# Optimization experiments

Hardware: AMD Instinct MI355X
Metric: run time of the kernel (lower is better)

The kernel has to match this reference:

```python
import jax, jax.numpy as jnp
import numpy as np

D_MODEL = 1024; D_STATE = 64; D_CONV = 4; EXPAND = 2; HEADDIM = 128; NGROUPS = 1; CHUNK = 256
D_INNER = EXPAND * D_MODEL            # 2048
NHEADS = D_INNER // HEADDIM           # 16
CONV_DIM = D_INNER + 2 * NGROUPS * D_STATE   # 2176
D_IN_PROJ = 2 * D_INNER + 2 * NGROUPS * D_STATE + NHEADS  # 4240
B = 4; G = 256; L = 2048
EPS = 1e-5


def setup_inputs() -> dict:
    key = jax.random.key(0)
    ks = jax.random.split(key, 12)
    def nrm(k, shape, s=0.02):
        return jax.random.normal(k, shape, jnp.float32) * s
    return dict(
        local_repr=jax.random.normal(ks[0], (B, L, D_MODEL), jnp.float32),
        global_repr=jax.random.normal(ks[1], (B, G, D_MODEL), jnp.float32),
        norm1_w=jnp.ones((D_MODEL,), jnp.float32), norm1_b=jnp.zeros((D_MODEL,), jnp.float32),
        norm2_w=jnp.ones((D_MODEL,), jnp.float32), norm2_b=jnp.zeros((D_MODEL,), jnp.float32),
        norm3_w=jnp.ones((D_MODEL,), jnp.float32), norm3_b=jnp.zeros((D_MODEL,), jnp.float32),
        in_proj_w=nrm(ks[2], (D_IN_PROJ, D_MODEL)),
        conv_w=nrm(ks[3], (CONV_DIM, D_CONV), 0.2),
        conv_b=jnp.zeros((CONV_DIM,), jnp.float32),
        dt_bias=jnp.log(jnp.expm1(jax.random.uniform(ks[4], (NHEADS,), jnp.float32, 1e-3, 0.1))),
        A_log=jnp.log(jax.random.uniform(ks[5], (NHEADS,), jnp.float32, 1.0, 16.0)),
        D_skip=jnp.ones((NHEADS,), jnp.float32),
        ssd_norm_w=jnp.ones((D_INNER,), jnp.float32),
        out_proj_w=nrm(ks[6], (D_MODEL, D_INNER)),
        ffn_w1=nrm(ks[7], (D_MODEL // 2, D_MODEL)),
        ffn_b1=jnp.zeros((D_MODEL // 2,), jnp.float32),
        ffn_w2=nrm(ks[8], (D_MODEL, D_MODEL // 2)),
        ffn_b2=jnp.zeros((D_MODEL,), jnp.float32),
    )


def _ln(x, w, b):
    mu = jnp.mean(x, axis=-1, keepdims=True)
    var = jnp.mean((x - mu) ** 2, axis=-1, keepdims=True)
    return (x - mu) * jax.lax.rsqrt(var + EPS) * w + b


def _segsum(a):
    # a: (..., T) -> (..., T, T) lower-triangular sums a[j+1..i]
    T = a.shape[-1]
    cs = jnp.cumsum(a, axis=-1)
    diff = cs[..., :, None] - cs[..., None, :]
    mask = jnp.tril(jnp.ones((T, T), bool))
    return jnp.where(mask, diff, -jnp.inf)


def _ssd(xdt, a_dt, Bh, Ch):
    # xdt: (b,t,h,p) = x*dt ; a_dt: (b,t,h) = dt*A ; Bh,Ch: (b,t,h,n)
    b, t, h, p = xdt.shape
    n = Bh.shape[-1]
    c = t // CHUNK
    X = xdt.reshape(b, c, CHUNK, h, p)
    Bc = Bh.reshape(b, c, CHUNK, h, n)
    Cc = Ch.reshape(b, c, CHUNK, h, n)
    Ac = a_dt.reshape(b, c, CHUNK, h).transpose(0, 3, 1, 2)  # (b,h,c,k)
    A_cum = jnp.cumsum(Ac, axis=-1)
    Lm = jnp.exp(_segsum(Ac))                                # (b,h,c,k,k)
    Y_diag = jnp.einsum('bckhn,bcshn,bhcks,bcshp->bckhp', Cc, Bc, Lm, X)
    decay_states = jnp.exp(A_cum[..., -1:] - A_cum)          # (b,h,c,k)
    states = jnp.einsum('bckhn,bhck,bckhp->bchpn', Bc, decay_states, X)
    A_last = jnp.pad(A_cum[..., -1], ((0, 0), (0, 0), (1, 0)))
    decay_chunk = jnp.exp(_segsum(A_last))                   # (b,h,c+1,c+1)
    states = jnp.concatenate([jnp.zeros_like(states[:, :1]), states], axis=1)
    new_states = jnp.einsum('bhzc,bchpn->bzhpn', decay_chunk, states)
    states_in = new_states[:, :-1]                           # (b,c,h,p,n)
    out_decay = jnp.exp(A_cum)                               # (b,h,c,k)
    Y_off = jnp.einsum('bckhn,bchpn,bhck->bckhp', Cc, states_in, out_decay)
    return (Y_diag + Y_off).reshape(b, t, h, p)


def _mamba2(x, in_proj_w, conv_w, conv_b, dt_bias, A_log, D_skip, ssd_norm_w, out_proj_w):
    b, t, _ = x.shape
    zxbcdt = x @ in_proj_w.T                                  # (b,t,D_IN_PROJ)
    z = zxbcdt[..., :D_INNER]
    xBC = zxbcdt[..., D_INNER:D_INNER + CONV_DIM]
    dt = jax.nn.softplus(zxbcdt[..., D_INNER + CONV_DIM:] + dt_bias)  # (b,t,h)
    # causal depthwise conv1d, kernel D_CONV
    xp = jnp.pad(xBC, ((0, 0), (D_CONV - 1, 0), (0, 0)))
    xBC = sum(xp[:, i:i + t, :] * conv_w[:, i] for i in range(D_CONV)) + conv_b
    xBC = jax.nn.silu(xBC)
    xs = xBC[..., :D_INNER].reshape(b, t, NHEADS, HEADDIM)
    Bm = xBC[..., D_INNER:D_INNER + NGROUPS * D_STATE].reshape(b, t, NGROUPS, D_STATE)
    Cm = xBC[..., D_INNER + NGROUPS * D_STATE:].reshape(b, t, NGROUPS, D_STATE)
    rep = NHEADS // NGROUPS
    Bh = jnp.repeat(Bm, rep, axis=2)
    Ch = jnp.repeat(Cm, rep, axis=2)
    A = -jnp.exp(A_log)                                       # (h,)
    Y = _ssd(xs * dt[..., None], dt * A, Bh, Ch)
    y = Y + D_skip[None, None, :, None] * xs
    y = y.reshape(b, t, D_INNER)
    # gated RMSNorm (norm_before_gate=False)
    y = y * jax.nn.silu(z)
    y = y * jax.lax.rsqrt(jnp.mean(y * y, axis=-1, keepdims=True) + EPS) * ssd_norm_w
    return y @ out_proj_w.T


def reference(local_repr, global_repr, norm1_w, norm1_b, norm2_w, norm2_b, norm3_w, norm3_b,
              in_proj_w, conv_w, conv_b, dt_bias, A_log, D_skip, ssd_norm_w, out_proj_w,
              ffn_w1, ffn_b1, ffn_w2, ffn_b2):
    local_n = _ln(local_repr, norm1_w, norm1_b)
    global_n = _ln(global_repr, norm2_w, norm2_b)
    x = jnp.concatenate([global_n, local_n], axis=1)          # (B, G+L, D)
    x = _mamba2(x, in_proj_w, conv_w, conv_b, dt_bias, A_log, D_skip, ssd_norm_w, out_proj_w)
    x = x[:, -local_n.shape[1]:, :] + local_n
    x = _ln(x, norm3_w, norm3_b)
    h = jax.nn.gelu(x @ ffn_w1.T + ffn_b1, approximate=False)
    return (h @ ffn_w2.T + ffn_b2) + x
```

## Files before the change

kernel.cpp:

```cpp
#include <hip/hip_runtime.h>
#include <math.h>

#define B_ 4
#define L_ 2048
#define G_ 256
#define T_ 2304
#define DM 1024
#define DINNER 2048
#define NH 16
#define HD 128
#define NSTATE 64
#define CONVD 2176
#define DPROJ 4240
#define NPROJ_PAD 4352
#define NCHUNK 9
#define CK 256
#define EPSV 1e-5f
#define CROWS 16
#define CONVBLKS 612

typedef unsigned short bf16t;
using bf16x8 = __attribute__((ext_vector_type(8))) short;
using f32x4  = __attribute__((ext_vector_type(4))) float;

__device__ __forceinline__ float bf2f(bf16t u) {
  return __uint_as_float(((unsigned int)u) << 16);
}
__device__ __forceinline__ bf16t f2bf(float f) {
  unsigned int u = __float_as_uint(f);
  u += 0x7FFFu + ((u >> 16) & 1u);
  return (bf16t)(u >> 16);
}

__device__ __forceinline__ void g2lds16(const bf16t* g, short* l) {
  __builtin_amdgcn_global_load_lds(
      (const __attribute__((address_space(1))) unsigned int*)g,
      (__attribute__((address_space(3))) unsigned int*)l, 16, 0, 0);
}

__device__ __forceinline__ int2 xcd_swz(int tiles_n) {
  int gx = gridDim.x, gy = gridDim.y;
  int id = blockIdx.y * gx + blockIdx.x;
  int cpx = (gx * gy) >> 3;
  int L = (id & 7) * cpx + (id >> 3);
  return make_int2(L % tiles_n, L / tiles_n);
}

__device__ __forceinline__ float2 block_reduce2(float a, float b) {
  __shared__ float sa[4], sb[4];
  #pragma unroll
  for (int off = 32; off > 0; off >>= 1) {
    a += __shfl_down(a, off, 64);
    b += __shfl_down(b, off, 64);
  }
  int lane = threadIdx.x & 63, wid = threadIdx.x >> 6;
  if (lane == 0) { sa[wid] = a; sb[wid] = b; }
  __syncthreads();
  return make_float2(sa[0] + sa[1] + sa[2] + sa[3], sb[0] + sb[1] + sb[2] + sb[3]);
}

__global__ __launch_bounds__(256) void ln_cvt_kernel(
    const float* __restrict__ localr, const float* __restrict__ globalr,
    const float* __restrict__ w1, const float* __restrict__ b1,
    const float* __restrict__ w2, const float* __restrict__ b2,
    bf16t* __restrict__ x, const float* __restrict__ inpw,
    bf16t* __restrict__ inpw_bf) {
  int blk = blockIdx.x;
  if (blk < B_ * T_) {
    int t = blk % T_, b = blk / T_;
    const float *src, *w, *bb;
    if (t < G_) { src = globalr + ((long)b * G_ + t) * DM;        w = w2; bb = b2; }
    else        { src = localr  + ((long)b * L_ + (t - G_)) * DM; w = w1; bb = b1; }
    int d = threadIdx.x * 4;
    float4 v = *(const float4*)&src[d];
    float s = v.x + v.y + v.z + v.w;
    float sq = v.x * v.x + v.y * v.y + v.z * v.z + v.w * v.w;
    float2 r2 = block_reduce2(s, sq);
    float mu = r2.x * (1.f / DM);
    float var = r2.y * (1.f / DM) - mu * mu;
    float rstd = rsqrtf(var + EPSV);
    float4 wv = *(const float4*)&w[d];
    float4 bv = *(const float4*)&bb[d];
    ushort4 o;
    o.x = f2bf((v.x - mu) * rstd * wv.x + bv.x);
    o.y = f2bf((v.y - mu) * rstd * wv.y + bv.y);
    o.z = f2bf((v.z - mu) * rstd * wv.z + bv.z);
    o.w = f2bf((v.w - mu) * rstd * wv.w + bv.w);
    *(ushort4*)&x[(long)blk * DM + d] = o;
  } else {
    long i = (long)(blk - B_ * T_) * 1024 + threadIdx.x * 4;
    const long nreal = (long)DPROJ * DM, ntot = (long)NPROJ_PAD * DM;
    if (i < ntot) {
      ushort4 o = {0, 0, 0, 0};
      if (i < nreal) {
        float4 v = *(const float4*)&inpw[i];
        o.x = f2bf(v.x); o.y = f2bf(v.y); o.z = f2bf(v.z); o.w = f2bf(v.w);
      }
      *(ushort4*)&inpw_bf[i] = o;
    }
  }
}

template<int EPI, bool OFFS, int K>
__global__ __launch_bounds__(512, 2) void gemm_wide(
    const bf16t* __restrict__ A, const bf16t* __restrict__ W,
    bf16t* __restrict__ Cb, bf16t* __restrict__ z, bf16t* __restrict__ xpre,
    float* __restrict__ dtr, const float* __restrict__ bias,
    const bf16t* __restrict__ res, float* __restrict__ Cf, int N) {
  __shared__ short LDS8[65536];
  int tid = threadIdx.x;
  int lane = tid & 63, w = tid >> 6;
  int wm = w >> 1, wn = w & 1;
  int l15 = lane & 15;
  int2 sz = xcd_swz(gridDim.x);
  int bn = sz.x * 128, bm = sz.y * 256;
  if (EPI == 0 && bn < DINNER && (bm % 2304) == 0) return;
  long bmA = OFFS ? ((long)(bm >> 11) * T_ + G_ + (bm & 2047)) : (long)bm;

  int csub = ((lane & 7) ^ (lane >> 3)) * 8;
  const bf16t* srcA = A + (bmA + w * 16 + (lane >> 3)) * (long)K + csub;
  const bf16t* srcW = W + (long)(bn + w * 16 + (lane >> 3)) * K + csub;
  int stageDst = w * 1024 + lane * 8;

  int off0 = l15 * 64 + (((lane >> 4) + 0) ^ (lane & 7)) * 8;
  int off1 = l15 * 64 + (((lane >> 4) + 4) ^ (lane & 7)) * 8;

  f32x4 acc[4][4] = {};
  bf16x8 af[2][2], bq[4][2];

#define STAGE2(gsrc, ldsoff) do { \
    g2lds16((gsrc), LDS8 + (ldsoff) + stageDst); \
    g2lds16((gsrc) + 8 * (long)K, LDS8 + (ldsoff) + stageDst + 512); } while (0)

  STAGE2(srcA, 0);
  STAGE2(srcA + 128 * (long)K, 8192);
  STAGE2(srcW, 49152);
  STAGE2(srcA + 64, 16384);
  STAGE2(srcA + 128 * (long)K + 64, 16384 + 8192);
  STAGE2(srcW + 64, 49152 + 8192);
  asm volatile("s_waitcnt vmcnt(6)" ::: "memory");
  __builtin_amdgcn_s_barrier();

  const int nt = K >> 6;
  for (int t = 0; t < nt; ++t) {
    int slotA = (t % 3) * 16384;
    int slotA2 = ((t + 2) % 3) * 16384;
    const short* aB = LDS8 + slotA + wm * 4096;
    const short* bB = LDS8 + 49152 + (t & 1) * 8192 + wn * 4096;

    #pragma unroll
    for (int mi = 0; mi < 2; mi++) {
      af[mi][0] = *(const bf16x8*)&aB[mi * 1024 + off0];
      af[mi][1] = *(const bf16x8*)&aB[mi * 1024 + off1];
    }
    #pragma unroll
    for (int ni = 0; ni < 2; ni++) {
      bq[ni][0] = *(const bf16x8*)&bB[ni * 1024 + off0];
      bq[ni][1] = *(const bf16x8*)&bB[ni * 1024 + off1];
    }
    if (t + 2 < nt) STAGE2(srcA + (t + 2) * 64, slotA2);
    __builtin_amdgcn_s_barrier();
    __builtin_amdgcn_s_setprio(1);
    #pragma unroll
    for (int ks = 0; ks < 2; ks++)
      #pragma unroll
      for (int mi = 0; mi < 2; mi++)
        #pragma unroll
        for (int ni = 0; ni < 2; ni++)
          acc[mi][ni] = __builtin_amdgcn_mfma_f32_16x16x32_bf16(af[mi][ks], bq[ni][ks], acc[mi][ni], 0, 0, 0);
    __builtin_amdgcn_s_setprio(0);
    __builtin_amdgcn_s_barrier();

    #pragma unroll
    for (int ni = 2; ni < 4; ni++) {
      bq[ni][0] = *(const bf16x8*)&bB[ni * 1024 + off0];
      bq[ni][1] = *(const bf16x8*)&bB[ni * 1024 + off1];
    }
    if (t + 2 < nt) STAGE2(srcA + 128 * (long)K + (t + 2) * 64, slotA2 + 8192);
    __builtin_amdgcn_s_barrier();
    __builtin_amdgcn_s_setprio(1);
    #pragma unroll
    for (int ks = 0; ks < 2; ks++)
      #pragma unroll
      for (int mi = 0; mi < 2; mi++)
        #pragma unroll
        for (int ni = 2; ni < 4; ni++)
          acc[mi][ni] = __builtin_amdgcn_mfma_f32_16x16x32_bf16(af[mi][ks], bq[ni][ks], acc[mi][ni], 0, 0, 0);
    __builtin_amdgcn_s_setprio(0);
    __builtin_amdgcn_s_barrier();

    #pragma unroll
    for (int mi = 0; mi < 2; mi++) {
      af[mi][0] = *(const bf16x8*)&aB[(mi + 2) * 1024 + off0];
      af[mi][1] = *(const bf16x8*)&aB[(mi + 2) * 1024 + off1];
    }
    if (t + 2 < nt) STAGE2(srcW + (t + 2) * 64, 49152 + (t & 1) * 8192);
    __builtin_amdgcn_s_barrier();
    __builtin_amdgcn_s_setprio(1);
    #pragma unroll
    for (int ks = 0; ks < 2; ks++)
      #pragma unroll
      for (int mi = 0; mi < 2; mi++)
        #pragma unroll
        for (int ni = 0; ni < 4; ni++)
          acc[mi + 2][ni] = __builtin_amdgcn_mfma_f32_16x16x32_bf16(af[mi][ks], bq[ni][ks], acc[mi + 2][ni], 0, 0, 0);
    __builtin_amdgcn_s_setprio(0);
    if (t + 2 < nt)      asm volatile("s_waitcnt vmcnt(6)" ::: "memory");
    else if (t + 1 < nt) asm volatile("s_waitcnt vmcnt(0)" ::: "memory");
    __builtin_amdgcn_s_barrier();
  }
#undef STAGE2

  if (EPI == 0 && bn == 4224) {
    if (wn == 0) {
      #pragma unroll
      for (int mi = 0; mi < 4; mi++)
        #pragma unroll
        for (int r = 0; r < 4; r++) {
          int row = bm + wm * 64 + mi * 16 + (lane >> 4) * 4 + r;
          dtr[(long)row * NH + l15] = acc[mi][0][r];
        }
    }
    return;
  }

  if (EPI == 2) {
    float* Cs32 = (float*)LDS8;
    #pragma unroll
    for (int pass = 0; pass < 2; pass++) {
      __syncthreads();
      if ((wm >> 1) == pass) {
        #pragma unroll
        for (int mi = 0; mi < 4; mi++)
          #pragma unroll
          for (int ni = 0; ni < 4; ni++)
            #pragma unroll
            for (int r = 0; r < 4; r++)
              Cs32[((wm & 1) * 64 + mi * 16 + (lane >> 4) * 4 + r) * 136 + wn * 64 + ni * 16 + l15] =
                  acc[mi][ni][r];
      }
      __syncthreads();
      #pragma unroll
      for (int q = 0; q < 4; q++) {
        int idx = q * 512 + tid;
        int row = idx >> 4, cg = (idx & 15) * 8;
        long grow = bm + pass * 128 + row; int gcol = bn + cg;
        float4 v0 = *(float4*)&Cs32[row * 136 + cg];
        float4 v1 = *(float4*)&Cs32[row * 136 + cg + 4];
        float4 b0 = *(const float4*)&bias[gcol];
        float4 b1 = *(const float4*)&bias[gcol + 4];
        bf16x8 rv = *(const bf16x8*)&res[grow * (long)N + gcol];
        v0.x += b0.x + bf2f((bf16t)rv[0]); v0.y += b0.y + bf2f((bf16t)rv[1]);
        v0.z += b0.z + bf2f((bf16t)rv[2]); v0.w += b0.w + bf2f((bf16t)rv[3]);
        v1.x += b1.x + bf2f((bf16t)rv[4]); v1.y += b1.y + bf2f((bf16t)rv[5]);
        v1.z += b1.z + bf2f((bf16t)rv[6]); v1.w += b1.w + bf2f((bf16t)rv[7]);
        *(float4*)&Cf[grow * (long)N + gcol] = v0;
        *(float4*)&Cf[grow * (long)N + gcol + 4] = v1;
      }
    }
    return;
  }

  bf16t* Cs = (bf16t*)LDS8;
  #pragma unroll
  for (int pass = 0; pass < 2; pass++) {
    __syncthreads();
    if ((wm >> 1) == pass) {
      #pragma unroll
      for (int mi = 0; mi < 4; mi++)
        #pragma unroll
        for (int ni = 0; ni < 4; ni++)
          #pragma unroll
          for (int r = 0; r < 4; r++)
            Cs[((wm & 1) * 64 + mi * 16 + (lane >> 4) * 4 + r) * 136 + wn * 64 + ni * 16 + l15] =
                f2bf(acc[mi][ni][r]);
    }
    __syncthreads();
    #pragma unroll
    for (int q = 0; q < 4; q++) {
      int idx = q * 512 + tid;
      int row = idx >> 4, cg = idx & 15;
      int gcol = bn + cg * 8;
      long grow = bm + pass * 128 + row;
      bf16x8 v = *(bf16x8*)&Cs[row * 136 + cg * 8];
      if (EPI == 0) {
        if (gcol < DINNER) *(bf16x8*)&z[grow * DINNER + gcol] = v;
        else               *(bf16x8*)&xpre[grow * CONVD + (gcol - DINNER)] = v;
      } else {
        *(bf16x8*)&Cb[grow * (long)N + gcol] = v;
      }
    }
  }
}

template<int EPI>
__global__ __launch_bounds__(256) void gemm_mfma(
    const bf16t* __restrict__ A, const bf16t* __restrict__ W,
    const float* __restrict__ bias, const bf16t* __restrict__ res,
    float* __restrict__ Cf, bf16t* __restrict__ Cb,
    int N, int K) {
  __shared__ __align__(16) short LDS[128 * 136];
  short* As = LDS;
  short* Ws = LDS + 128 * 32;
  int tid = threadIdx.x;
  int lane = tid & 63, w = tid >> 6;
  int wr = w >> 1, wc = w & 1;
  int2 sz = xcd_swz(gridDim.x);
  int bn = sz.x * 128, bm = sz.y * 128;

  int r1 = tid >> 2,         s1 = (((tid & 3) ^ ((r1 >> 1) & 3))) * 8;
  int r2 = (tid + 256) >> 2, s2 = (((tid & 3) ^ ((r2 >> 1) & 3))) * 8;
  const bf16t* gA1 = A + (long)(bm + r1) * K + s1;
  const bf16t* gA2 = A + (long)(bm + r2) * K + s2;
  const bf16t* gW1 = W + (long)(bn + r1) * K + s1;
  const bf16t* gW2 = W + (long)(bn + r2) * K + s2;
  short* lA1 = As + tid * 8;
  short* lA2 = As + (tid + 256) * 8;
  short* lW1 = Ws + tid * 8;
  short* lW2 = Ws + (tid + 256) * 8;

  int arow = wr * 64 + (lane & 15);
  int brow = wc * 64 + (lane & 15);
  int koff = (((lane >> 4) ^ (((lane & 15) >> 1) & 3))) * 8;

  f32x4 acc[4][4] = {};
  for (int k0 = 0; k0 < K; k0 += 32) {
    g2lds16(gA1 + k0, lA1);
    g2lds16(gA2 + k0, lA2);
    g2lds16(gW1 + k0, lW1);
    g2lds16(gW2 + k0, lW2);
    __syncthreads();
    bf16x8 af[4], bf[4];
    #pragma unroll
    for (int mi = 0; mi < 4; mi++) af[mi] = *(bf16x8*)&As[(arow + mi * 16) * 32 + koff];
    #pragma unroll
    for (int ni = 0; ni < 4; ni++) bf[ni] = *(bf16x8*)&Ws[(brow + ni * 16) * 32 + koff];
    #pragma unroll
    for (int mi = 0; mi < 4; mi++)
      #pragma unroll
      for (int ni = 0; ni < 4; ni++)
        acc[mi][ni] = __builtin_amdgcn_mfma_f32_16x16x32_bf16(af[mi], bf[ni], acc[mi][ni], 0, 0, 0);
    __syncthreads();
  }

  int rb = wr * 64 + (lane >> 4) * 4;
  int cb = wc * 64 + (lane & 15);

  __syncthreads();
  bf16t* Cs = (bf16t*)LDS;
  #pragma unroll
  for (int mi = 0; mi < 4; mi++)
    #pragma unroll
    for (int ni = 0; ni < 4; ni++)
      #pragma unroll
      for (int r = 0; r < 4; r++) {
        float v = acc[mi][ni][r];
        if (EPI == 2) {
          v += bias[bn + cb + ni * 16];
          v = 0.5f * v * (1.f + erff(v * 0.70710678118f));
        }
        Cs[(rb + mi * 16 + r) * 136 + cb + ni * 16] = f2bf(v);
      }
  __syncthreads();
  #pragma unroll
  for (int pass = 0; pass < 8; pass++) {
    int row = pass * 16 + (tid >> 4);
    int col = (tid & 15) * 8;
    bf16x8 vv = *(bf16x8*)&Cs[row * 136 + col];
    long grow = bm + row; int gcol = bn + col;
    *(bf16x8*)&Cb[grow * N + gcol] = vv;
  }
}

__global__ __launch_bounds__(256) void conv_cumsum_kernel(
    const bf16t* __restrict__ xpre, const float* __restrict__ cw,
    const float* __restrict__ cb, bf16t* __restrict__ out,
    const float* __restrict__ dtraw, const float* __restrict__ dt_bias,
    const float* __restrict__ A_log, float* __restrict__ dt,
    float* __restrict__ Acum) {
  if (blockIdx.x < CONVBLKS) {
    int gt = blockIdx.x * 256 + threadIdx.x;
    int cg = gt % 272; int rt = gt / 272;
    int c0 = cg * 8;
    long r0 = (long)rt * CROWS;
    int t0 = (int)(r0 % T_);

    float wreg[4][8];
    #pragma unroll
    for (int j = 0; j < 8; j++) {
      float4 wa = *(const float4*)&cw[(c0 + j) * 4];
      wreg[0][j] = wa.x; wreg[1][j] = wa.y; wreg[2][j] = wa.z; wreg[3][j] = wa.w;
    }
    float4 cb0 = *(const float4*)&cb[c0];
    float4 cb1 = *(const float4*)&cb[c0 + 4];
    float bias[8] = {cb0.x, cb0.y, cb0.z, cb0.w, cb1.x, cb1.y, cb1.z, cb1.w};

    bf16x8 win[4];
    #pragma unroll
    for (int i = 0; i < 3; i++) {
      if (t0 - 3 + i >= 0) win[i] = *(const bf16x8*)&xpre[(r0 - 3 + i) * CONVD + c0];
      else                 win[i] = bf16x8{0,0,0,0,0,0,0,0};
    }

    #pragma unroll
    for (int k = 0; k < CROWS; k++) {
      win[3] = *(const bf16x8*)&xpre[(r0 + k) * CONVD + c0];
      float acc[8];
      #pragma unroll
      for (int j = 0; j < 8; j++) acc[j] = bias[j];
      #pragma unroll
      for (int i = 0; i < 4; i++)
        #pragma unroll
        for (int j = 0; j < 8; j++)
          acc[j] += bf2f((bf16t)win[i][j]) * wreg[i][j];
      bf16x8 o;
      #pragma unroll
      for (int j = 0; j < 8; j++) {
        float s = acc[j] / (1.f + __expf(-acc[j]));
        o[j] = (short)f2bf(s);
      }
      *(bf16x8*)&out[(r0 + k) * CONVD + c0] = o;
      win[0] = win[1]; win[1] = win[2]; win[2] = win[3];
    }
  } else {
    int bid = blockIdx.x - CONVBLKS;
    int c = bid % NCHUNK; int hh = bid / NCHUNK;
    int h = hh % NH; int b = hh / NH;
    int k = threadIdx.x;
    float a = -__expf(A_log[h]);
    long t = (long)b * T_ + c * CK + k;
    float v0 = dtraw[t * NH + h] + dt_bias[h];
    float dtv = (v0 > 20.f) ? v0 : log1pf(__expf(v0));
    dt[t * NH + h] = dtv;
    float v = dtv * a;
    __shared__ float buf[2][CK];
    int cur = 0;
    buf[0][k] = v; __syncthreads();
    for (int off = 1; off < CK; off <<= 1) {
      float tv = buf[cur][k];
      if (k >= off) tv += buf[cur][k - off];
      buf[1 - cur][k] = tv; cur ^= 1; __syncthreads();
    }
    Acum[(long)bid * CK + k] = buf[cur][k];
  }
}

__global__ __launch_bounds__(256) void chunk_states_kernel(
    const bf16t* __restrict__ xbc, const float* __restrict__ dt,
    const float* __restrict__ Acum, float* __restrict__ cs) {
  int bid = blockIdx.x;
  int h = bid & 15; int bc = bid >> 4;
  int c = bc & 7; int b = bc >> 3;
  int tid = threadIdx.x;
  int lane = tid & 63, w = tid >> 6;
  long tch = (long)b * T_ + c * CK;
  int acb = ((b * NH + h) * NCHUNK + c) * CK;
  float Alast = Acum[acb + CK - 1];

  __shared__ bf16t Xt[128][72];
  __shared__ bf16t Bt[64][72];
  __shared__ float wk[64];

  f32x4 acc[8] = {};
  for (int kb = 0; kb < 4; kb++) {
    int s0 = kb * 64;
    __syncthreads();
    if (tid < 64)
      wk[tid] = __expf(Alast - Acum[acb + s0 + tid]) * dt[(tch + s0 + tid) * NH + h];
    __syncthreads();
    for (int e = tid; e < 16 * 32; e += 256) {
      int s4 = (e & 15) * 4, p4 = e >> 4;
      const bf16t* base = &xbc[(tch + s0 + s4) * CONVD + h * HD + p4 * 4];
      ushort4 u0 = *(const ushort4*)(base);
      ushort4 u1 = *(const ushort4*)(base + CONVD);
      ushort4 u2 = *(const ushort4*)(base + 2 * CONVD);
      ushort4 u3 = *(const ushort4*)(base + 3 * CONVD);
      float w0 = wk[s4], w1 = wk[s4 + 1], w2 = wk[s4 + 2], w3 = wk[s4 + 3];
      ushort4 pk;
      pk.x = f2bf(bf2f(u0.x) * w0); pk.y = f2bf(bf2f(u1.x) * w1);
      pk.z = f2bf(bf2f(u2.x) * w2); pk.w = f2bf(bf2f(u3.x) * w3);
      *(ushort4*)&Xt[p4 * 4 + 0][s4] = pk;
      pk.x = f2bf(bf2f(u0.y) * w0); pk.y = f2bf(bf2f(u1.y) * w1);
      pk.z = f2bf(bf2f(u2.y) * w2); pk.w = f2bf(bf2f(u3.y) * w3);
      *(ushort4*)&Xt[p4 * 4 + 1][s4] = pk;
      pk.x = f2bf(bf2f(u0.z) * w0); pk.y = f2bf(bf2f(u1.z) * w1);
      pk.z = f2bf(bf2f(u2.z) * w2); pk.w = f2bf(bf2f(u3.z) * w3);
      *(ushort4*)&Xt[p4 * 4 + 2][s4] = pk;
      pk.x = f2bf(bf2f(u0.w) * w0); pk.y = f2bf(bf2f(u1.w) * w1);
      pk.z = f2bf(bf2f(u2.w) * w2); pk.w = f2bf(bf2f(u3.w) * w3);
      *(ushort4*)&Xt[p4 * 4 + 3][s4] = pk;
    }
    for (int e = tid; e < 16 * 16; e += 256) {
      int s4 = (e & 15) * 4, n4 = e >> 4;
      const bf16t* base = &xbc[(tch + s0 + s4) * CONVD + DINNER + n4 * 4];
      ushort4 u0 = *(const ushort4*)(base);
      ushort4 u1 = *(const ushort4*)(base + CONVD);
      ushort4 u2 = *(const ushort4*)(base + 2 * CONVD);
      ushort4 u3 = *(const ushort4*)(base + 3 * CONVD);
      ushort4 pk;
      pk.x = u0.x; pk.y = u1.x; pk.z = u2.x; pk.w = u3.x;
      *(ushort4*)&Bt[n4 * 4 + 0][s4] = pk;
      pk.x = u0.y; pk.y = u1.y; pk.z = u2.y; pk.w = u3.y;
      *(ushort4*)&Bt[n4 * 4 + 1][s4] = pk;
      pk.x = u0.z; pk.y = u1.z; pk.z = u2.z; pk.w = u3.z;
      *(ushort4*)&Bt[n4 * 4 + 2][s4] = pk;
      pk.x = u0.w; pk.y = u1.w; pk.z = u2.w; pk.w = u3.w;
      *(ushort4*)&Bt[n4 * 4 + 3][s4] = pk;
    }
    __syncthreads();
    #pragma unroll
    for (int ks = 0; ks < 2; ks++) {
      int koff = (lane >> 4) * 8 + ks * 32;
      bf16x8 bfr = *(bf16x8*)&Bt[w * 16 + (lane & 15)][koff];
      #pragma unroll
      for (int mi = 0; mi < 8; mi++) {
        bf16x8 af = *(bf16x8*)&Xt[mi * 16 + (lane & 15)][koff];
        acc[mi] = __builtin_amdgcn_mfma_f32_16x16x32_bf16(af, bfr, acc[mi], 0, 0, 0);
      }
    }
  }
  int cbid = (b * NCHUNK + c) * NH + h;
  float* out = cs + (long)cbid * HD * NSTATE;
  int n = w * 16 + (lane & 15);
  #pragma unroll
  for (int mi = 0; mi < 8; mi++) {
    #pragma unroll
    for (int r = 0; r < 4; r++) {
      int p = mi * 16 + (lane >> 4) * 4 + r;
      out[p * NSTATE + n] = acc[mi][r];
    }
  }
}

__global__ __launch_bounds__(256) void state_pass_kernel(
    float* __restrict__ cs, const float* __restrict__ Acum) {
  int bh = blockIdx.x;
  int b = bh / NH, h = bh % NH;
  int e0 = blockIdx.y * 1024 + threadIdx.x;
  for (int q = 0; q < 4; q++) {
    int e = e0 + q * 256;
    float s = 0.f;
    for (int c = 0; c < NCHUNK; c++) {
      long idx = ((long)(b * NCHUNK + c) * NH + h) * (HD * NSTATE) + e;
      if (c < NCHUNK - 1) {
        float tmp = cs[idx];
        cs[idx] = s;
        float g = __expf(Acum[((b * NH + h) * NCHUNK + c) * CK + CK - 1]);
        s = s * g + tmp;
      } else {
        cs[idx] = s;
      }
    }
  }
}

__global__ __launch_bounds__(256) void ssd_y_kernel(
    const bf16t* __restrict__ xbc, const float* __restrict__ dt,
    const float* __restrict__ Acum, const float* __restrict__ sin_,
    const float* __restrict__ Dskip, bf16t* __restrict__ Y) {
  int bid = blockIdx.x;
  int h = bid & 15; int bc = bid >> 4;
  int c = 1 + (bc & 7); int b = bc >> 3;
  int rt = blockIdx.y;
  int tid = threadIdx.x;
  int lane = tid & 63, w = tid >> 6;
  int wr = w >> 1, wc = w & 1;
  long tch = (long)b * T_ + c * CK;
  long tbase = tch + rt * 128;
  int acb = ((b * NH + h) * NCHUNK + c) * CK;

  __shared__ bf16t Cs[128][72];
  __shared__ bf16t Bs[64][72];
  __shared__ __align__(16) bf16t XtSm[2][128][72];
  bf16t (*Xt)[72] = XtSm[0];
  bf16t (*Sm)[72] = XtSm[1];
  __shared__ float Akl[128];
  __shared__ float Asl[64];
  __shared__ float dts[64];

  for (int e = tid; e < 128 * 8; e += 256) {
    int row = e >> 3, seg = (e & 7) * 8;
    *(bf16x8*)&Cs[row][seg] =
        *(const bf16x8*)&xbc[(tbase + row) * CONVD + DINNER + NSTATE + seg];
  }
  if (tid < 128) Akl[tid] = Acum[acb + rt * 128 + tid];

  f32x4 acc[4][4] = {};
  int nsb = 2 * (rt + 1);
  for (int sb = 0; sb < nsb; sb++) {
    int s0 = sb * 64;
    __syncthreads();
    if (tid < 64) {
      Asl[tid] = Acum[acb + s0 + tid];
      dts[tid] = dt[(tch + s0 + tid) * NH + h];
    }
    __syncthreads();
    for (int e = tid; e < 64 * 8; e += 256) {
      int row = e >> 3, seg = (e & 7) * 8;
      *(bf16x8*)&Bs[row][seg] =
          *(const bf16x8*)&xbc[(tch + s0 + row) * CONVD + DINNER + seg];
    }
    for (int e = tid; e < 16 * 32; e += 256) {
      int s4 = (e & 15) * 4, p4 = e >> 4;
      const bf16t* base = &xbc[(tch + s0 + s4) * CONVD + h * HD + p4 * 4];
      ushort4 u0 = *(const ushort4*)(base);
      ushort4 u1 = *(const ushort4*)(base + CONVD);
      ushort4 u2 = *(const ushort4*)(base + 2 * CONVD);
      ushort4 u3 = *(const ushort4*)(base + 3 * CONVD);
      float d0 = dts[s4], d1 = dts[s4 + 1], d2 = dts[s4 + 2], d3 = dts[s4 + 3];
      ushort4 pk;
      pk.x = f2bf(bf2f(u0.x) * d0); pk.y = f2bf(bf2f(u1.x) * d1);
      pk.z = f2bf(bf2f(u2.x) * d2); pk.w = f2bf(bf2f(u3.x) * d3);
      *(ushort4*)&Xt[p4 * 4 + 0][s4] = pk;
      pk.x = f2bf(bf2f(u0.y) * d0); pk.y = f2bf(bf2f(u1.y) * d1);
      pk.z = f2bf(bf2f(u2.y) * d2); pk.w = f2bf(bf2f(u3.y) * d3);
      *(ushort4*)&Xt[p4 * 4 + 1][s4] = pk;
      pk.x = f2bf(bf2f(u0.z) * d0); pk.y = f2bf(bf2f(u1.z) * d1);
      pk.z = f2bf(bf2f(u2.z) * d2); pk.w = f2bf(bf2f(u3.z) * d3);
      *(ushort4*)&Xt[p4 * 4 + 2][s4] = pk;
      pk.x = f2bf(bf2f(u0.w) * d0); pk.y = f2bf(bf2f(u1.w) * d1);
      pk.z = f2bf(bf2f(u2.w) * d2); pk.w = f2bf(bf2f(u3.w) * d3);
      *(ushort4*)&Xt[p4 * 4 + 3][s4] = pk;
    }
    __syncthreads();
    {
      f32x4 sacc[2][4] = {};
      int rw0 = w * 32;
      #pragma unroll
      for (int ks = 0; ks < 2; ks++) {
        int koff = (lane >> 4) * 8 + ks * 32;
        bf16x8 a0 = *(bf16x8*)&Cs[rw0 + (lane & 15)][koff];
        bf16x8 a1 = *(bf16x8*)&Cs[rw0 + 16 + (lane & 15)][koff];
        #pragma unroll
        for (int ni = 0; ni < 4; ni++) {
          bf16x8 bfr = *(bf16x8*)&Bs[ni * 16 + (lane & 15)][koff];
          sacc[0][ni] = __builtin_amdgcn_mfma_f32_16x16x32_bf16(a0, bfr, sacc[0][ni], 0, 0, 0);
          sacc[1][ni] = __builtin_amdgcn_mfma_f32_16x16x32_bf16(a1, bfr, sacc[1][ni], 0, 0, 0);
        }
      }
      #pragma unroll
      for (int mi = 0; mi < 2; mi++) {
        #pragma unroll
        for (int ni = 0; ni < 4; ni++) {
          #pragma unroll
          for (int r = 0; r < 4; r++) {
            int row = rw0 + mi * 16 + (lane >> 4) * 4 + r;
            int scol = ni * 16 + (lane & 15);
            int kglob = rt * 128 + row;
            int sglob = s0 + scol;
            float val = 0.f;
            if (sglob <= kglob) val = sacc[mi][ni][r] * __expf(Akl[row] - Asl[scol]);
            Sm[row][scol] = f2bf(val);
          }
        }
      }
    }
    __syncthreads();
    #pragma unroll
    for (int ks = 0; ks < 2; ks++) {
      int koff = (lane >> 4) * 8 + ks * 32;
      bf16x8 af[4], bfr[4];
      #pragma unroll
      for (int mi = 0; mi < 4; mi++) af[mi] = *(bf16x8*)&Sm[wr * 64 + mi * 16 + (lane & 15)][koff];
      #pragma unroll
      for (int ni = 0; ni < 4; ni++) bfr[ni] = *(bf16x8*)&Xt[wc * 64 + ni * 16 + (lane & 15)][koff];
      #pragma unroll
      for (int mi = 0; mi < 4; mi++)
        #pragma unroll
        for (int ni = 0; ni < 4; ni++)
          acc[mi][ni] = __builtin_amdgcn_mfma_f32_16x16x32_bf16(af[mi], bfr[ni], acc[mi][ni], 0, 0, 0);
    }
  }

  float ekr[16];
  #pragma unroll
  for (int mi = 0; mi < 4; mi++)
    #pragma unroll
    for (int r = 0; r < 4; r++)
      ekr[mi * 4 + r] = __expf(Akl[wr * 64 + mi * 16 + (lane >> 4) * 4 + r]);

  int cbid = (b * NCHUNK + c) * NH + h;
  const float* sinb = sin_ + (long)cbid * HD * NSTATE;
  #pragma unroll
  for (int ni = 0; ni < 4; ni++) {
    f32x4 offacc[4] = {};
    int p = wc * 64 + ni * 16 + (lane & 15);
    #pragma unroll
    for (int ks = 0; ks < 2; ks++) {
      int koff = (lane >> 4) * 8 + ks * 32;
      const float* srow = sinb + p * NSTATE + koff;
      float4 sa = *(const float4*)srow;
      float4 sbv = *(const float4*)(srow + 4);
      bf16x8 bfr;
      bfr[0] = (short)f2bf(sa.x);  bfr[1] = (short)f2bf(sa.y);
      bfr[2] = (short)f2bf(sa.z);  bfr[3] = (short)f2bf(sa.w);
      bfr[4] = (short)f2bf(sbv.x); bfr[5] = (short)f2bf(sbv.y);
      bfr[6] = (short)f2bf(sbv.z); bfr[7] = (short)f2bf(sbv.w);
      #pragma unroll
      for (int mi = 0; mi < 4; mi++) {
        bf16x8 af = *(bf16x8*)&Cs[wr * 64 + mi * 16 + (lane & 15)][koff];
        offacc[mi] = __builtin_amdgcn_mfma_f32_16x16x32_bf16(af, bfr, offacc[mi], 0, 0, 0);
      }
    }
    #pragma unroll
    for (int mi = 0; mi < 4; mi++)
      #pragma unroll
      for (int r = 0; r < 4; r++)
        acc[mi][ni][r] += ekr[mi * 4 + r] * offacc[mi][r];
  }

  float dsk = Dskip[h];
  float* Sf = (float*)&XtSm[0][0][0];
  #pragma unroll
  for (int rh = 0; rh < 2; rh++) {
    __syncthreads();
    if (wr == rh) {
      #pragma unroll
      for (int mi = 0; mi < 4; mi++)
        #pragma unroll
        for (int ni = 0; ni < 4; ni++)
          #pragma unroll
          for (int r = 0; r < 4; r++)
            Sf[(mi * 16 + (lane >> 4) * 4 + r) * 130 + wc * 64 + ni * 16 + (lane & 15)] =
                acc[mi][ni][r];
    }
    __syncthreads();
    #pragma unroll
    for (int g = 0; g < 4; g++) {
      int idx = g * 256 + tid;
      int row = idx >> 4, cg = (idx & 15) * 8;
      long t = tbase + rh * 64 + row;
      bf16x8 xv = *(const bf16x8*)&xbc[t * CONVD + h * HD + cg];
      bf16x8 o;
      #pragma unroll
      for (int j = 0; j < 8; j++)
        o[j] = (short)f2bf(Sf[row * 130 + cg + j] + dsk * bf2f((bf16t)xv[j]));
      *(bf16x8*)&Y[t * DINNER + h * HD + cg] = o;
    }
  }
}

__global__ __launch_bounds__(256) void gate_rms_cvt_kernel(
    const bf16t* __restrict__ z, const float* __restrict__ nw,
    bf16t* __restrict__ Y,
    const float* __restrict__ outw, const float* __restrict__ f1w,
    const float* __restrict__ f2w, bf16t* __restrict__ o_out,
    bf16t* __restrict__ o_f1, bf16t* __restrict__ o_f2) {
  int blk = blockIdx.x;
  if (blk < B_ * L_) {
    long r = (long)(blk >> 11) * T_ + G_ + (blk & 2047);
    const bf16t* zrow = z + r * DINNER;
    bf16t* yrow = Y + r * DINNER;
    int tid = threadIdx.x;
    int d = tid * 8;
    bf16x8 zu = *(const bf16x8*)&zrow[d];
    bf16x8 yu = *(const bf16x8*)&yrow[d];
    float v[8]; float sq = 0.f;
    #pragma unroll
    for (int j = 0; j < 8; j++) {
      float z0 = bf2f((bf16t)zu[j]);
      float y0 = bf2f((bf16t)yu[j]) * (z0 / (1.f + __expf(-z0)));
      v[j] = y0; sq += y0 * y0;
    }
    float2 r2 = block_reduce2(sq, 0.f);
    float rms = rsqrtf(r2.x * (1.f / DINNER) + EPSV);
    float4 nw0 = *(const float4*)&nw[d];
    float4 nw1 = *(const float4*)&nw[d + 4];
    float nn[8] = {nw0.x, nw0.y, nw0.z, nw0.w, nw1.x, nw1.y, nw1.z, nw1.w};
    bf16x8 o;
    #pragma unroll
    for (int j = 0; j < 8; j++) o[j] = (short)f2bf(v[j] * rms * nn[j]);
    *(bf16x8*)&yrow[d] = o;
  } else {
    long i = (long)(blk - B_ * L_) * 1024 + threadIdx.x * 4;
    const long n1 = (long)DM * DINNER;
    const long n2 = (long)(DM / 2) * DM;
    const float* src; bf16t* dst; long off;
    if (i < n1) { src = outw; dst = o_out; off = i; }
    else if (i < n1 + n2) { src = f1w; dst = o_f1; off = i - n1; }
    else { src = f2w; dst = o_f2; off = i - n1 - n2; }
    float4 v = *(const float4*)&src[off];
    ushort4 o;
    o.x = f2bf(v.x); o.y = f2bf(v.y); o.z = f2bf(v.z); o.w = f2bf(v.w);
    *(ushort4*)&dst[off] = o;
  }
}

__global__ __launch_bounds__(256) void res_ln3_kernel(
    const bf16t* __restrict__ mfull, const bf16t* __restrict__ x,
    const float* __restrict__ w3, const float* __restrict__ b3,
    bf16t* __restrict__ x2) {
  int rl = blockIdx.x;
  int tl = rl & 2047, b = rl >> 11;
  long rt = (long)b * T_ + G_ + tl;
  const bf16t* m = mfull + (long)rl * DM;
  const bf16t* xr = x + rt * DM;
  int tid = threadIdx.x;
  int d = tid * 4;
  ushort4 mu4 = *(const ushort4*)&m[d];
  ushort4 xu4 = *(const ushort4*)&xr[d];
  float v[4];
  v[0] = bf2f(mu4.x) + bf2f(xu4.x);
  v[1] = bf2f(mu4.y) + bf2f(xu4.y);
  v[2] = bf2f(mu4.z) + bf2f(xu4.z);
  v[3] = bf2f(mu4.w) + bf2f(xu4.w);
  float s = v[0] + v[1] + v[2] + v[3];
  float sq = v[0]*v[0] + v[1]*v[1] + v[2]*v[2] + v[3]*v[3];
  float2 r2 = block_reduce2(s, sq);
  float mu = r2.x * (1.f / DM);
  float var = r2.y * (1.f / DM) - mu * mu;
  float rstd = rsqrtf(var + EPSV);
  float4 w4 = *(const float4*)&w3[d];
  float4 b4 = *(const float4*)&b3[d];
  ushort4 o;
  o.x = f2bf((v[0] - mu) * rstd * w4.x + b4.x);
  o.y = f2bf((v[1] - mu) * rstd * w4.y + b4.y);
  o.z = f2bf((v[2] - mu) * rstd * w4.z + b4.z);
  o.w = f2bf((v[3] - mu) * rstd * w4.w + b4.w);
  *(ushort4*)&x2[(long)rl * DM + d] = o;
}

extern "C" void kernel_launch(void* const* d_in, const int* in_sizes, int n_in,
                              void* d_out, int out_size, void* d_ws, size_t ws_size,
                              hipStream_t stream) {
  const float* localr = (const float*)d_in[0];
  const float* globalr= (const float*)d_in[1];
  const float* n1w = (const float*)d_in[2];
  const float* n1b = (const float*)d_in[3];
  const float* n2w = (const float*)d_in[4];
  const float* n2b = (const float*)d_in[5];
  const float* n3w = (const float*)d_in[6];
  const float* n3b = (const float*)d_in[7];
  const float* inpw= (const float*)d_in[8];
  const float* convw=(const float*)d_in[9];
  const float* convb=(const float*)d_in[10];
  const float* dtb = (const float*)d_in[11];
  const float* alog= (const float*)d_in[12];
  const float* dskp= (const float*)d_in[13];
  const float* ssdw= (const float*)d_in[14];
  const float* outw= (const float*)d_in[15];
  const float* f1w = (const float*)d_in[16];
  const float* f1b = (const float*)d_in[17];
  const float* f2w = (const float*)d_in[18];
  const float* f2b = (const float*)d_in[19];

  char* ws = (char*)d_ws;
  bf16t* x     = (bf16t*)(ws + 0);
  bf16t* z     = (bf16t*)(ws + 18874368);
  bf16t* mfull = (bf16t*)(ws + 18874368);
  bf16t* xpre  = (bf16t*)(ws + 56623104);
  bf16t* Yb    = (bf16t*)(ws + 56623104);
  float* dtraw = (float*)(ws + 96731136);
  float* dt    = (float*)(ws + 97320960);
  float* Acum  = (float*)(ws + 97910784);
  bf16t* xbc   = (bf16t*)(ws + 98500608);
  bf16t* x2bf  = (bf16t*)(ws + 98500608);
  bf16t* hbuf  = (bf16t*)(ws + 115277824);
  bf16t* outw_bf = (bf16t*)(ws + 123666432);
  bf16t* f1w_bf  = (bf16t*)(ws + 127860736);
  bf16t* f2w_bf  = (bf16t*)(ws + 128909312);
  float* cs    = (float*)(ws + 138608640);
  bf16t* inpw_bf = (bf16t*)(ws + 138608640);

  ln_cvt_kernel<<<B_ * T_ + 4352, 256, 0, stream>>>(
      localr, globalr, n1w, n1b, n2w, n2b, x, inpw, inpw_bf);

  gemm_wide<0, false, 1024><<<dim3(NPROJ_PAD / 128, (B_ * T_) / 256), 512, 0, stream>>>(
      x, inpw_bf, nullptr, z, xpre, dtraw, nullptr, nullptr, nullptr, NPROJ_PAD);

  conv_cumsum_kernel<<<CONVBLKS + B_ * NH * NCHUNK, 256, 0, stream>>>(
      xpre, convw, convb, xbc, dtraw, dtb, alog, dt, Acum);

  chunk_states_kernel<<<B_ * (NCHUNK - 1) * NH, 256, 0, stream>>>(xbc, dt, Acum, cs);

  state_pass_kernel<<<dim3(B_ * NH, 8), 256, 0, stream>>>(cs, Acum);

  ssd_y_kernel<<<dim3(B_ * (NCHUNK - 1) * NH, 2), 256, 0, stream>>>(
      xbc, dt, Acum, cs, dskp, Yb);

  gate_rms_cvt_kernel<<<B_ * L_ + 3072, 256, 0, stream>>>(
      z, ssdw, Yb, outw, f1w, f2w, outw_bf, f1w_bf, f2w_bf);

  gemm_wide<1, true, 2048><<<dim3(DM / 128, (B_ * L_) / 256), 512, 0, stream>>>(
      Yb, outw_bf, mfull, nullptr, nullptr, nullptr, nullptr, nullptr, nullptr, DM);

  res_ln3_kernel<<<B_ * L_, 256, 0, stream>>>(mfull, x, n3w, n3b, x2bf);

  gemm_mfma<2><<<dim3((DM / 2) / 128, (B_ * L_) / 128), 256, 0, stream>>>(
      x2bf, f1w_bf, f1b, nullptr, nullptr, hbuf, DM / 2, DM);

  gemm_wide<2, false, 512><<<dim3(DM / 128, (B_ * L_) / 256), 512, 0, stream>>>(
      hbuf, f2w_bf, nullptr, nullptr, nullptr, nullptr, f2b, x2bf, (float*)d_out, DM);
}
```

Before: 450.0 us.

## Halve GEMM K-tile to shrink LDS, raise occupancy, hoist per-chunk scalars

The wide GEMM now stages 32-wide K slices instead of 64, with a triple-buffered ring for both A and W. This cuts the LDS footprint from 128KB to 72KB and the launch bound is raised to 4 blocks per SM, which should improve latency hiding. The cost is twice as many loop iterations and barriers, and the fp32 epilogue now needs four passes. Separately, the chunk-state and chunk-scan kernels load all 256 Acum/dt values (and the exp weights) into LDS once up front, removing a per-sub-block barrier and reload.

```diff
diff --git a/kernel.cpp b/kernel.cpp
--- a/kernel.cpp
+++ b/kernel.cpp
@@ -102,12 +102,12 @@
 }
 
 template<int EPI, bool OFFS, int K>
-__global__ __launch_bounds__(512, 2) void gemm_wide(
+__global__ __launch_bounds__(512, 4) void gemm_wide(
     const bf16t* __restrict__ A, const bf16t* __restrict__ W,
     bf16t* __restrict__ Cb, bf16t* __restrict__ z, bf16t* __restrict__ xpre,
     float* __restrict__ dtr, const float* __restrict__ bias,
     const bf16t* __restrict__ res, float* __restrict__ Cf, int N) {
-  __shared__ short LDS8[65536];
+  __shared__ short LDS8[36864];
   int tid = threadIdx.x;
   int lane = tid & 63, w = tid >> 6;
   int wm = w >> 1, wn = w & 1;
@@ -117,99 +117,67 @@
   if (EPI == 0 && bn < DINNER && (bm % 2304) == 0) return;
   long bmA = OFFS ? ((long)(bm >> 11) * T_ + G_ + (bm & 2047)) : (long)bm;
 
-  int csub = ((lane & 7) ^ (lane >> 3)) * 8;
-  const bf16t* srcA = A + (bmA + w * 16 + (lane >> 3)) * (long)K + csub;
-  const bf16t* srcW = W + (long)(bn + w * 16 + (lane >> 3)) * K + csub;
-  int stageDst = w * 1024 + lane * 8;
-
-  int off0 = l15 * 64 + (((lane >> 4) + 0) ^ (lane & 7)) * 8;
-  int off1 = l15 * 64 + (((lane >> 4) + 4) ^ (lane & 7)) * 8;
+  int csub = ((lane & 3) ^ ((lane >> 2) & 3)) * 8;
+  const bf16t* srcA = A + (bmA + w * 16 + (lane >> 2)) * (long)K + csub;
+  const bf16t* srcW = W + (long)(bn + w * 16 + (lane >> 2)) * K + csub;
+  int stageDst = w * 512 + lane * 8;
+
+  int off0 = l15 * 32 + ((lane >> 4) ^ (l15 & 3)) * 8;
 
   f32x4 acc[4][4] = {};
-  bf16x8 af[2][2], bq[4][2];
-
-#define STAGE2(gsrc, ldsoff) do { \
+  bf16x8 af[4], bq[4];
+
+#define STAGEA(gsrc, ldsoff) do { \
     g2lds16((gsrc), LDS8 + (ldsoff) + stageDst); \
-    g2lds16((gsrc) + 8 * (long)K, LDS8 + (ldsoff) + stageDst + 512); } while (0)
-
-  STAGE2(srcA, 0);
-  STAGE2(srcA + 128 * (long)K, 8192);
-  STAGE2(srcW, 49152);
-  STAGE2(srcA + 64, 16384);
-  STAGE2(srcA + 128 * (long)K + 64, 16384 + 8192);
-  STAGE2(srcW + 64, 49152 + 8192);
-  asm volatile("s_waitcnt vmcnt(6)" ::: "memory");
+    g2lds16((gsrc) + 128 * (long)K, LDS8 + (ldsoff) + stageDst + 4096); } while (0)
+#define STAGEB(gsrc, ldsoff) g2lds16((gsrc), LDS8 + (ldsoff) + stageDst)
+
+  STAGEA(srcA, 0);
+  STAGEB(srcW, 24576);
+  STAGEA(srcA + 32, 8192);
+  STAGEB(srcW + 32, 24576 + 4096);
+  asm volatile("s_waitcnt vmcnt(3)" ::: "memory");
   __builtin_amdgcn_s_barrier();
 
-  const int nt = K >> 6;
+  const int nt = K >> 5;
   for (int t = 0; t < nt; ++t) {
-    int slotA = (t % 3) * 16384;
-    int slotA2 = ((t + 2) % 3) * 16384;
-    const short* aB = LDS8 + slotA + wm * 4096;
-    const short* bB = LDS8 + 49152 + (t & 1) * 8192 + wn * 4096;
-
-    #pragma unroll
-    for (int mi = 0; mi < 2; mi++) {
-      af[mi][0] = *(const bf16x8*)&aB[mi * 1024 + off0];
-      af[mi][1] = *(const bf16x8*)&aB[mi * 1024 + off1];
-    }
-    #pragma unroll
-    for (int ni = 0; ni < 2; ni++) {
-      bq[ni][0] = *(const bf16x8*)&bB[ni * 1024 + off0];
-      bq[ni][1] = *(const bf16x8*)&bB[ni * 1024 + off1];
-    }
-    if (t + 2 < nt) STAGE2(srcA + (t + 2) * 64, slotA2);
+    const short* aB = LDS8 + (t % 3) * 8192 + wm * 2048;
+    const short* bB = LDS8 + 24576 + (t % 3) * 4096 + wn * 2048;
+    int nsA = ((t + 2) % 3) * 8192;
+    int nsB = 24576 + ((t + 2) % 3) * 4096;
+
+    #pragma unroll
+    for (int mi = 0; mi < 4; mi++) af[mi] = *(const bf16x8*)&aB[mi * 512 + off0];
+    #pragma unroll
+    for (int ni = 0; ni < 2; ni++) bq[ni] = *(const bf16x8*)&bB[ni * 512 + off0];
+    if (t + 2 < nt) STAGEA(srcA + (t + 2) * 32, nsA);
     __builtin_amdgcn_s_barrier();
     __builtin_amdgcn_s_setprio(1);
     #pragma unroll
-    for (int ks = 0; ks < 2; ks++)
-      #pragma unroll
-      for (int mi = 0; mi < 2; mi++)
-        #pragma unroll
-        for (int ni = 0; ni < 2; ni++)
-          acc[mi][ni] = __builtin_amdgcn_mfma_f32_16x16x32_bf16(af[mi][ks], bq[ni][ks], acc[mi][ni], 0, 0, 0);
+    for (int mi = 0; mi < 4; mi++)
+      #pragma unroll
+      for (int ni = 0; ni < 2; ni++)
+        acc[mi][ni] = __builtin_amdgcn_mfma_f32_16x16x32_bf16(af[mi], bq[ni], acc[mi][ni], 0, 0, 0);
     __builtin_amdgcn_s_setprio(0);
     __builtin_amdgcn_s_barrier();
 
     #pragma unroll
-    for (int ni = 2; ni < 4; ni++) {
-      bq[ni][0] = *(const bf16x8*)&bB[ni * 1024 + off0];
-      bq[ni][1] = *(const bf16x8*)&bB[ni * 1024 + off1];
-    }
-    if (t + 2 < nt) STAGE2(srcA + 128 * (long)K + (t + 2) * 64, slotA2 + 8192);
+    for (int ni = 2; ni < 4; ni++) bq[ni] = *(const bf16x8*)&bB[ni * 512 + off0];
+    if (t + 2 < nt) STAGEB(srcW + (t + 2) * 32, nsB);
     __builtin_amdgcn_s_barrier();
     __builtin_amdgcn_s_setprio(1);
     #pragma unroll
-    for (int ks = 0; ks < 2; ks++)
-      #pragma unroll
-      for (int mi = 0; mi < 2; mi++)
-        #pragma unroll
-        for (int ni = 2; ni < 4; ni++)
-          acc[mi][ni] = __builtin_amdgcn_mfma_f32_16x16x32_bf16(af[mi][ks], bq[ni][ks], acc[mi][ni], 0, 0, 0);
+    for (int mi = 0; mi < 4; mi++)
+      #pragma unroll
+      for (int ni = 2; ni < 4; ni++)
+        acc[mi][ni] = __builtin_amdgcn_mfma_f32_16x16x32_bf16(af[mi], bq[ni], acc[mi][ni], 0, 0, 0);
     __builtin_amdgcn_s_setprio(0);
-    __builtin_amdgcn_s_barrier();
-
-    #pragma unroll
-    for (int mi = 0; mi < 2; mi++) {
-      af[mi][0] = *(const bf16x8*)&aB[(mi + 2) * 1024 + off0];
-      af[mi][1] = *(const bf16x8*)&aB[(mi + 2) * 1024 + off1];
-    }
-    if (t + 2 < nt) STAGE2(srcW + (t + 2) * 64, 49152 + (t & 1) * 8192);
-    __builtin_amdgcn_s_barrier();
-    __builtin_amdgcn_s_setprio(1);
-    #pragma unroll
-    for (int ks = 0; ks < 2; ks++)
-      #pragma unroll
-      for (int mi = 0; mi < 2; mi++)
-        #pragma unroll
-        for (int ni = 0; ni < 4; ni++)
-          acc[mi + 2][ni] = __builtin_amdgcn_mfma_f32_16x16x32_bf16(af[mi][ks], bq[ni][ks], acc[mi + 2][ni], 0, 0, 0);
-    __builtin_amdgcn_s_setprio(0);
-    if (t + 2 < nt)      asm volatile("s_waitcnt vmcnt(6)" ::: "memory");
+    if (t + 2 < nt)      asm volatile("s_waitcnt vmcnt(3)" ::: "memory");
     else if (t + 1 < nt) asm volatile("s_waitcnt vmcnt(0)" ::: "memory");
     __builtin_amdgcn_s_barrier();
   }
-#undef STAGE2
+#undef STAGEA
+#undef STAGEB
 
   if (EPI == 0 && bn == 4224) {
     if (wn == 0) {
@@ -227,24 +195,24 @@
   if (EPI == 2) {
     float* Cs32 = (float*)LDS8;
     #pragma unroll
-    for (int pass = 0; pass < 2; pass++) {
+    for (int pass = 0; pass < 4; pass++) {
       __syncthreads();
-      if ((wm >> 1) == pass) {
+      if (wm == pass) {
         #pragma unroll
         for (int mi = 0; mi < 4; mi++)
           #pragma unroll
           for (int ni = 0; ni < 4; ni++)
             #pragma unroll
             for (int r = 0; r < 4; r++)
-              Cs32[((wm & 1) * 64 + mi * 16 + (lane >> 4) * 4 + r) * 136 + wn * 64 + ni * 16 + l15] =
+              Cs32[(mi * 16 + (lane >> 4) * 4 + r) * 136 + wn * 64 + ni * 16 + l15] =
                   acc[mi][ni][r];
       }
       __syncthreads();
       #pragma unroll
-      for (int q = 0; q < 4; q++) {
+      for (int q = 0; q < 2; q++) {
         int idx = q * 512 + tid;
         int row = idx >> 4, cg = (idx & 15) * 8;
-        long grow = bm + pass * 128 + row; int gcol = bn + cg;
+        long grow = bm + pass * 64 + row; int gcol = bn + cg;
         float4 v0 = *(float4*)&Cs32[row * 136 + cg];
         float4 v1 = *(float4*)&Cs32[row * 136 + cg + 4];
         float4 b0 = *(const float4*)&bias[gcol];
@@ -459,14 +427,12 @@
 
   __shared__ bf16t Xt[128][72];
   __shared__ bf16t Bt[64][72];
-  __shared__ float wk[64];
+  __shared__ float wkv[256];
+  wkv[tid] = __expf(Alast - Acum[acb + tid]) * dt[(tch + tid) * NH + h];
 
   f32x4 acc[8] = {};
   for (int kb = 0; kb < 4; kb++) {
     int s0 = kb * 64;
-    __syncthreads();
-    if (tid < 64)
-      wk[tid] = __expf(Alast - Acum[acb + s0 + tid]) * dt[(tch + s0 + tid) * NH + h];
     __syncthreads();
     for (int e = tid; e < 16 * 32; e += 256) {
       int s4 = (e & 15) * 4, p4 = e >> 4;
@@ -475,7 +441,8 @@
       ushort4 u1 = *(const ushort4*)(base + CONVD);
       ushort4 u2 = *(const ushort4*)(base + 2 * CONVD);
       ushort4 u3 = *(const ushort4*)(base + 3 * CONVD);
-      float w0 = wk[s4], w1 = wk[s4 + 1], w2 = wk[s4 + 2], w3 = wk[s4 + 3];
+      float w0 = wkv[s0 + s4], w1 = wkv[s0 + s4 + 1];
+      float w2 = wkv[s0 + s4 + 2], w3 = wkv[s0 + s4 + 3];
       ushort4 pk;
       pk.x = f2bf(bf2f(u0.x) * w0); pk.y = f2bf(bf2f(u1.x) * w1);
       pk.z = f2bf(bf2f(u2.x) * w2); pk.w = f2bf(bf2f(u3.x) * w3);
@@ -574,26 +541,22 @@
   __shared__ __align__(16) bf16t XtSm[2][128][72];
   bf16t (*Xt)[72] = XtSm[0];
   bf16t (*Sm)[72] = XtSm[1];
-  __shared__ float Akl[128];
-  __shared__ float Asl[64];
-  __shared__ float dts[64];
+  __shared__ float Acv[256];
+  __shared__ float dtv[256];
 
   for (int e = tid; e < 128 * 8; e += 256) {
     int row = e >> 3, seg = (e & 7) * 8;
     *(bf16x8*)&Cs[row][seg] =
         *(const bf16x8*)&xbc[(tbase + row) * CONVD + DINNER + NSTATE + seg];
   }
-  if (tid < 128) Akl[tid] = Acum[acb + rt * 128 + tid];
+  Acv[tid] = Acum[acb + tid];
+  dtv[tid] = dt[(tch + tid) * NH + h];
+  const float* Ak = Acv + rt * 128;
 
   f32x4 acc[4][4] = {};
   int nsb = 2 * (rt + 1);
   for (int sb = 0; sb < nsb; sb++) {
     int s0 = sb * 64;
-    __syncthreads();
-    if (tid < 64) {
-      Asl[tid] = Acum[acb + s0 + tid];
-      dts[tid] = dt[(tch + s0 + tid) * NH + h];
-    }
     __syncthreads();
     for (int e = tid; e < 64 * 8; e += 256) {
       int row = e >> 3, seg = (e & 7) * 8;
@@ -607,7 +570,8 @@
       ushort4 u1 = *(const ushort4*)(base + CONVD);
       ushort4 u2 = *(const ushort4*)(base + 2 * CONVD);
       ushort4 u3 = *(const ushort4*)(base + 3 * CONVD);
-      float d0 = dts[s4], d1 = dts[s4 + 1], d2 = dts[s4 + 2], d3 = dts[s4 + 3];
+      float d0 = dtv[s0 + s4], d1 = dtv[s0 + s4 + 1];
+      float d2 = dtv[s0 + s4 + 2], d3 = dtv[s0 + s4 + 3];
       ushort4 pk;
       pk.x = f2bf(bf2f(u0.x) * d0); pk.y = f2bf(bf2f(u1.x) * d1);
       pk.z = f2bf(bf2f(u2.x) * d2); pk.w = f2bf(bf2f(u3.x) * d3);
@@ -649,7 +613,7 @@
             int kglob = rt * 128 + row;
             int sglob = s0 + scol;
             float val = 0.f;
-            if (sglob <= kglob) val = sacc[mi][ni][r] * __expf(Akl[row] - Asl[scol]);
+            if (sglob <= kglob) val = sacc[mi][ni][r] * __expf(Ak[row] - Acv[s0 + scol]);
             Sm[row][scol] = f2bf(val);
           }
         }
@@ -677,7 +641,7 @@
   for (int mi = 0; mi < 4; mi++)
     #pragma unroll
     for (int r = 0; r < 4; r++)
-      ekr[mi * 4 + r] = __expf(Akl[wr * 64 + mi * 16 + (lane >> 4) * 4 + r]);
+      ekr[mi * 4 + r] = __expf(Ak[wr * 64 + mi * 16 + (lane >> 4) * 4 + r]);
 
   int cbid = (b * NCHUNK + c) * NH + h;
   const float* sinb = sin_ + (long)cbid * HD * NSTATE;
```

After: 459.3 us. +2.1%, slower.
